# Kernel optimization log

Hardware: AMD Instinct MI355X
Metric: run time of the kernel (lower is better)

## Reference

```python
import jax, jax.numpy as jnp
import numpy as np

B, S, D, H, T = 512, 256, 64, 256, 50
IN = 2 * D + 1  # LSTM input dim = input_size*2+1
NSUB = 8       # RK4 substeps per output interval
TIME_OFFSET = 0.0

def _xavier(k, shape):
    fan_out, fan_in = shape
    lim = float(np.sqrt(6.0 / (fan_in + fan_out)))
    return jax.random.uniform(k, shape, minval=-lim, maxval=lim, dtype=jnp.float32)

def setup_inputs() -> dict:
    key = jax.random.key(0)
    ks = jax.random.split(key, 12)
    gaps = jax.random.uniform(ks[3], (B, T), minval=0.05, maxval=0.2, dtype=jnp.float32)
    return {
        "x": jax.random.normal(ks[0], (B, S, IN), jnp.float32),
        "lengths": jax.random.randint(ks[1], (B,), S // 2, S + 1),
        "label_feature": jax.random.normal(ks[2], (B, T, D), jnp.float32),
        "label_time": jnp.cumsum(gaps, axis=1),  # sorted per-sample times
        "label_mask": (jax.random.uniform(ks[4], (B, T, D)) < 0.2).astype(jnp.float32),
        "W_ih": _xavier(ks[5], (4 * H, IN)),
        "W_hh": _xavier(ks[6], (4 * H, H)),
        "b_ih": jnp.zeros((4 * H,), jnp.float32),
        "b_hh": jnp.zeros((4 * H,), jnp.float32),
        "Wp1": _xavier(ks[7], (H, H)), "bp1": jnp.zeros((H,), jnp.float32),
        "Wp2": _xavier(ks[8], (D, H)), "bp2": jnp.zeros((D,), jnp.float32),
        "Wd1": _xavier(ks[9], (H, D)), "bd1": jnp.zeros((H,), jnp.float32),
        "Wd2": _xavier(ks[10], (D, H)), "bd2": jnp.zeros((D,), jnp.float32),
    }

def _forward(x, label_feature, label_time, label_mask,
             W_ih, W_hh, b_ih, b_hh, Wp1, bp1, Wp2, bp2, Wd1, bd1, Wd2, bd2,
             lengths):
    # --- LSTM encoder (PyTorch gate order i, f, g, o) ---
    xW = jnp.einsum('bsi,gi->bsg', x, W_ih) + b_ih  # [B,S,4H]
    h0 = jnp.zeros((x.shape[0], H), x.dtype)
    def step(carry, xt):
        h, c = carry
        g = xt + h @ W_hh.T + b_hh
        i, f, gg, o = jnp.split(g, 4, axis=-1)
        c = jax.nn.sigmoid(f) * c + jax.nn.sigmoid(i) * jnp.tanh(gg)
        h = jax.nn.sigmoid(o) * jnp.tanh(c)
        return (h, c), h
    _, hs = jax.lax.scan(step, (h0, h0), jnp.swapaxes(xW, 0, 1))
    hs = jnp.swapaxes(hs, 0, 1)  # [B,S,H]
    # masked mean over valid timesteps
    mask = (jnp.arange(x.shape[1])[None, :] < lengths[:, None]).astype(x.dtype)
    pooled = (hs * mask[:, :, None]).sum(axis=1) / lengths[:, None].astype(x.dtype)
    # projection MLP -> initial ODE state
    y0 = jax.nn.relu(pooled @ Wp1.T + bp1) @ Wp2.T + bp2  # [B,D]
    # --- batched Neural-ODE integration (fixed-step RK4) ---
    def deriv(y):
        return jax.nn.relu(y @ Wd1.T + bd1) @ Wd2.T + bd2
    ts = label_time - TIME_OFFSET
    dts = (ts[:, 1:] - ts[:, :-1]) / NSUB  # [B,T-1]
    def interval(y, dt_b):
        dt = dt_b[:, None]
        for _ in range(NSUB):
            k1 = deriv(y)
            k2 = deriv(y + 0.5 * dt * k1)
            k3 = deriv(y + 0.5 * dt * k2)
            k4 = deriv(y + dt * k3)
            y = y + (dt / 6.0) * (k1 + 2.0 * k2 + 2.0 * k3 + k4)
        return y, y
    _, traj = jax.lax.scan(interval, y0, jnp.swapaxes(dts, 0, 1))  # [T-1,B,D]
    predict = jnp.swapaxes(jnp.concatenate([y0[None], traj], axis=0), 0, 1)  # [B,T,D]
    loss = (predict - label_feature) ** 2 * (1.0 - label_mask)
    return predict, loss

def reference(x, lengths, label_feature, label_time, label_mask,
              W_ih, W_hh, b_ih, b_hh, Wp1, bp1, Wp2, bp2, Wd1, bd1, Wd2, bd2):
    return _forward(x, label_feature, label_time, label_mask,
                    W_ih, W_hh, b_ih, b_hh, Wp1, bp1, Wp2, bp2, Wd1, bd1, Wd2, bd2,
                    lengths)
```

## Files before the change

kernel.cpp:

```cpp
#include <hip/hip_runtime.h>
#include <hip/hip_bf16.h>

#define BB 512
#define SS 256
#define HH 256
#define DD 64
#define TT 50
#define GG 1024
#define INW 129

typedef _Float16 h4 __attribute__((ext_vector_type(4)));
typedef _Float16 h8 __attribute__((ext_vector_type(8)));
typedef __fp16 hf2 __attribute__((ext_vector_type(2)));
typedef float f32x4 __attribute__((ext_vector_type(4)));
typedef unsigned int u32;

__device__ inline float sigf(float x) { return 1.f / (1.f + __expf(-x)); }
__device__ inline float tanhf_(float x) { return 1.f - 2.f / (__expf(2.f * x) + 1.f); }

__device__ inline u32 pkrtz(float a, float b) {
    hf2 h = __builtin_amdgcn_cvt_pkrtz(a, b);
    return __builtin_bit_cast(u32, h);
}
__device__ inline float fdot2u(u32 a, u32 b, float c) {
    return __builtin_amdgcn_fdot2(__builtin_bit_cast(hf2, a), __builtin_bit_cast(hf2, b), c, false);
}

__global__ __launch_bounds__(256) void prep_kernel(
    const float* __restrict__ W_hh, const float* __restrict__ W_ih,
    const float* __restrict__ Wd1, const float* __restrict__ Wd2,
    h4* __restrict__ BhhV4, h4* __restrict__ BhhL4, h4* __restrict__ BhhS4,
    _Float16* __restrict__ Bih, u32* __restrict__ Wd1p, u32* __restrict__ Wd2p)
{
    int idx = blockIdx.x * 256 + threadIdx.x;
    if (idx < 65536) {
        int eh = idx & 1;
        int l = (idx >> 1) & 63;
        int ks = (idx >> 7) & 7;
        int s = (idx >> 10) & 7;
        int w = (idx >> 13) & 7;
        int g = s & 3, jt = s >> 2;
        int n = g * 256 + w * 32 + jt * 16 + (l & 15);
        int k = 32 * ks + 8 * (l >> 4) + 4 * eh;
        float4 v = *(const float4*)(W_hh + (size_t)n * HH + k);
        h4 o; o[0] = (_Float16)v.x; o[1] = (_Float16)v.y; o[2] = (_Float16)v.z; o[3] = (_Float16)v.w;
        if (ks < 4)      BhhV4[(((w * 8 + s) * 4 + ks) * 64 + l) * 2 + eh] = o;
        else if (ks < 6) BhhL4[(((w * 8 + s) * 2 + (ks - 4)) * 64 + l) * 2 + eh] = o;
        else             BhhS4[(((w * 8 + s) * 2 + (ks - 6)) * 64 + l) * 2 + eh] = o;
    } else if (idx < 65536 + 40960) {
        int fj = idx - 65536;
        int eh = fj & 1;
        int l = (fj >> 1) & 63;
        int si = fj >> 7;
        int ks = si % 5;
        int ntile = si / 5;
        int n = ntile * 16 + (l & 15);
        int k = 32 * ks + 8 * (l >> 4) + 4 * eh;
        h4 o;
#pragma unroll
        for (int i = 0; i < 4; i++) {
            int kk = k + i;
            o[i] = (_Float16)((kk < INW) ? W_ih[(size_t)n * INW + kk] : 0.f);
        }
        *(h4*)(Bih + (size_t)fj * 4) = o;
    } else if (idx < 106496 + 8192) {
        int j2 = idx - 106496;
        int j = j2 >> 8, i = j2 & 255;
        Wd1p[j2] = pkrtz(Wd1[i * DD + 2 * j], Wd1[i * DD + 2 * j + 1]);
    } else if (idx < 114688 + 8192) {
        int j2 = idx - 114688;
        int j = j2 >> 8, t = j2 & 255;
        int o = ((t >> 6) << 4) + (t & 15);
        int q = (t >> 4) & 3;
        Wd2p[j2] = pkrtz(Wd2[(size_t)o * HH + q * 64 + 2 * j],
                         Wd2[(size_t)o * HH + q * 64 + 2 * j + 1]);
    }
}

__global__ __launch_bounds__(256) void xw_kernel(
    const float* __restrict__ x, const _Float16* __restrict__ Bih,
    const float* __restrict__ b_ih, const float* __restrict__ b_hh,
    h4* __restrict__ xwf)
{
    __shared__ __align__(16) _Float16 ash[4][5][64][8];
    int tid = threadIdx.x;
    int w4 = tid >> 6, l = tid & 63;
    int bx = blockIdx.x;
    int t = bx >> 3, Bb = bx & 7;

    for (int i = tid; i < 64 * 160; i += 256) {
        int rr = i / 160, kk = i % 160;
        float v = (kk < INW) ? x[((size_t)(Bb * 64 + rr) * SS + t) * INW + kk] : 0.f;
        ash[rr >> 4][kk >> 5][(((kk & 31) >> 3) << 4) + (rr & 15)][kk & 7] = (_Float16)v;
    }
    __syncthreads();

    h8 A[4][5];
#pragma unroll
    for (int ms = 0; ms < 4; ms++)
#pragma unroll
        for (int ks = 0; ks < 5; ks++)
            A[ms][ks] = *(h8*)&ash[ms][ks][l][0];

    const h8* Bih8 = (const h8*)Bih;
    for (int nt16 = 0; nt16 < 16; nt16++) {
        int ntile = w4 * 16 + nt16;
        h8 Bv[5];
#pragma unroll
        for (int ks = 0; ks < 5; ks++) Bv[ks] = Bih8[(ntile * 5 + ks) * 64 + l];
        int nb = ntile * 16 + (l & 15);
        float bias = b_ih[nb] + b_hh[nb];
        f32x4 acc[4];
#pragma unroll
        for (int ms = 0; ms < 4; ms++) acc[ms] = (f32x4){0.f, 0.f, 0.f, 0.f};
#pragma unroll
        for (int ks = 0; ks < 5; ks++)
#pragma unroll
            for (int ms = 0; ms < 4; ms++)
                acc[ms] = __builtin_amdgcn_mfma_f32_16x16x32_f16(A[ms][ks], Bv[ks], acc[ms], 0, 0, 0);
        int slot = ((ntile & 15) >> 1) * 8 + (ntile & 1) * 4 + (ntile >> 4);
#pragma unroll
        for (int ms = 0; ms < 4; ms++) {
            int bg = Bb * 4 + ms;
            h4 o;
#pragma unroll
            for (int r = 0; r < 4; r++) o[r] = (_Float16)(acc[ms][r] + bias);
            xwf[(((size_t)bg * SS + t) * 64 + slot) * 64 + l] = o;
        }
    }
}

__global__ __launch_bounds__(512, 2) void lstm_kernel(
    const h8* __restrict__ BhhV, const h8* __restrict__ BhhL, const h8* __restrict__ BhhS,
    const h4* __restrict__ xwf, const int* __restrict__ lengths, float* __restrict__ pooled)
{
    __shared__ __align__(16) _Float16 Wlds[65536];
    __shared__ __align__(16) _Float16 hbuf[2][8][64][8];
    int tid = threadIdx.x;
    int w = tid >> 6, l = tid & 63;
    int bg = blockIdx.x;

    {
        const uint4* src = (const uint4*)BhhL;
        uint4* dst = (uint4*)Wlds;
#pragma unroll
        for (int i = 0; i < 16; i++) dst[i * 512 + tid] = src[i * 512 + tid];
    }

    h8 Wv[8][4];
#pragma unroll
    for (int s = 0; s < 8; s++)
#pragma unroll
        for (int ks = 0; ks < 4; ks++)
            Wv[s][ks] = BhhV[((w * 8 + s) * 4 + ks) * 64 + l];

    int len_[4];
    float c_[2][4], pa[2][4];
#pragma unroll
    for (int r = 0; r < 4; r++) {
        int b = 4 * (l >> 4) + r;
        len_[r] = lengths[bg * 16 + b];
#pragma unroll
        for (int jt = 0; jt < 2; jt++) { c_[jt][r] = 0.f; pa[jt][r] = 0.f; }
    }

    {
        uint4* hz = (uint4*)hbuf;
        hz[tid] = make_uint4(0, 0, 0, 0);
        hz[512 + tid] = make_uint4(0, 0, 0, 0);
    }
    __syncthreads();

    int cur = 0;
    for (int t = 0; t < SS; t++) {
        const h4* xpb = xwf + (((size_t)bg * SS + t) * 64 + w * 8) * 64 + l;
        int zoff = 0;
        asm volatile("" : "+v"(zoff));
        const h8* bS = BhhS + zoff;
#pragma unroll
        for (int jt = 0; jt < 2; jt++) {
            h4 xv[4];
#pragma unroll
            for (int g = 0; g < 4; g++) xv[g] = xpb[(jt * 4 + g) * 64];
            h8 Ws[4];
#pragma unroll
            for (int g = 0; g < 4; g++) Ws[g] = bS[((w * 8 + jt * 4 + g) * 2 + 0) * 64 + l];
            f32x4 acc[4];
#pragma unroll
            for (int g = 0; g < 4; g++) acc[g] = (f32x4){0.f, 0.f, 0.f, 0.f};
#pragma unroll
            for (int ks = 0; ks < 4; ks++) {
                h8 A = *(const h8*)&hbuf[cur][ks][l][0];
#pragma unroll
                for (int g = 0; g < 4; g++)
                    acc[g] = __builtin_amdgcn_mfma_f32_16x16x32_f16(A, Wv[jt * 4 + g][ks], acc[g], 0, 0, 0);
            }
            {
                h8 A = *(const h8*)&hbuf[cur][6][l][0];
#pragma unroll
                for (int g = 0; g < 4; g++)
                    acc[g] = __builtin_amdgcn_mfma_f32_16x16x32_f16(A, Ws[g], acc[g], 0, 0, 0);
            }
#pragma unroll
            for (int g = 0; g < 4; g++) Ws[g] = bS[((w * 8 + jt * 4 + g) * 2 + 1) * 64 + l];
#pragma unroll
            for (int ks = 4; ks < 6; ks++) {
                h8 A = *(const h8*)&hbuf[cur][ks][l][0];
#pragma unroll
                for (int g = 0; g < 4; g++) {
                    h8 Bw = *(const h8*)&Wlds[(((w * 8 + jt * 4 + g) * 2 + (ks - 4)) * 64 + l) * 8];
                    acc[g] = __builtin_amdgcn_mfma_f32_16x16x32_f16(A, Bw, acc[g], 0, 0, 0);
                }
            }
            {
                h8 A = *(const h8*)&hbuf[cur][7][l][0];
#pragma unroll
                for (int g = 0; g < 4; g++)
                    acc[g] = __builtin_amdgcn_mfma_f32_16x16x32_f16(A, Ws[g], acc[g], 0, 0, 0);
            }
#pragma unroll
            for (int r = 0; r < 4; r++) {
                float gi = acc[0][r] + (float)xv[0][r];
                float gf = acc[1][r] + (float)xv[1][r];
                float gg = acc[2][r] + (float)xv[2][r];
                float go = acc[3][r] + (float)xv[3][r];
                float cc = sigf(gf) * c_[jt][r] + sigf(gi) * tanhf_(gg);
                c_[jt][r] = cc;
                float hh = sigf(go) * tanhf_(cc);
                if (t < len_[r]) pa[jt][r] += hh;
                int b = 4 * (l >> 4) + r;
                int j = w * 32 + jt * 16 + (l & 15);
                hbuf[cur ^ 1][j >> 5][(((j & 31) >> 3) << 4) + b][j & 7] = (_Float16)hh;
            }
        }
        __syncthreads();
        cur ^= 1;
    }

#pragma unroll
    for (int jt = 0; jt < 2; jt++)
#pragma unroll
        for (int r = 0; r < 4; r++) {
            int b = 4 * (l >> 4) + r;
            int j = w * 32 + jt * 16 + (l & 15);
            pooled[(size_t)(bg * 16 + b) * HH + j] = pa[jt][r] / (float)len_[r];
        }
}

__global__ __launch_bounds__(256) void head_kernel(
    const float* __restrict__ pooled, const float* __restrict__ Wp1,
    const float* __restrict__ bp1, const float* __restrict__ Wp2,
    const float* __restrict__ bp2, float* __restrict__ y0ws)
{
    __shared__ __align__(16) float psh[HH];
    __shared__ __align__(16) float rsh[HH];
    int tid = threadIdx.x, b = blockIdx.x;
    psh[tid] = pooled[(size_t)b * HH + tid];
    __syncthreads();
    float a = bp1[tid];
    const float* wr = Wp1 + (size_t)tid * HH;
#pragma unroll 8
    for (int k = 0; k < HH; k += 4) {
        float4 w = *(const float4*)(wr + k);
        a += psh[k] * w.x + psh[k + 1] * w.y + psh[k + 2] * w.z + psh[k + 3] * w.w;
    }
    rsh[tid] = fmaxf(a, 0.f);
    __syncthreads();
    if (tid < DD) {
        float acc = bp2[tid];
        const float* w2 = Wp2 + (size_t)tid * HH;
#pragma unroll 8
        for (int h = 0; h < HH; h += 4) {
            float4 w = *(const float4*)(w2 + h);
            acc += rsh[h] * w.x + rsh[h + 1] * w.y + rsh[h + 2] * w.z + rsh[h + 3] * w.w;
        }
        y0ws[(size_t)b * DD + tid] = acc;
    }
}

__global__ __launch_bounds__(256) void ode_kernel(
    const float* __restrict__ y0ws, const u32* __restrict__ Wd1p,
    const float* __restrict__ bd1, const u32* __restrict__ Wd2p,
    const float* __restrict__ bd2, const float* __restrict__ ltime,
    const float* __restrict__ lfeat, const float* __restrict__ lmask,
    float* __restrict__ pred, float* __restrict__ losso)
{
    __shared__ __align__(16) u32 ysh16[32];
    __shared__ __align__(16) u32 hsh16[128];
    int tid = threadIdx.x;
    int wv = tid >> 6, lq = tid & 63;
    int o = (wv << 4) + (lq & 15), q = lq >> 4;
    int b = blockIdx.x;
    u32 w1p[32], w2p[32];
#pragma unroll
    for (int j = 0; j < 32; j++) w1p[j] = Wd1p[j * 256 + tid];
#pragma unroll
    for (int j = 0; j < 32; j++) w2p[j] = Wd2p[j * 256 + tid];
    float bd1t = bd1[tid];
    float bd2o = bd2[o];
    float y = y0ws[(size_t)b * DD + o];
    if (q == 0) {
        size_t idx = ((size_t)b * TT + 0) * DD + o;
        pred[idx] = y;
        float lf = lfeat[idx], lm = lmask[idx];
        losso[idx] = (y - lf) * (y - lf) * (1.f - lm);
    }
    float kp = 0.f;
    for (int iv = 0; iv < TT - 1; iv++) {
        float t0 = ltime[(size_t)b * TT + iv], t1 = ltime[(size_t)b * TT + iv + 1];
        float dt = (t1 - t0) * 0.125f;
        for (int ss = 0; ss < 8; ss++) {
            float sacc = 0.f;
            kp = 0.f;
            const float AE[4] = {0.f, 0.5f, 0.5f, 1.f};
            const float WE[4] = {1.f, 2.f, 2.f, 1.f};
#pragma unroll
            for (int e = 0; e < 4; e++) {
                float yp = y + AE[e] * dt * kp;
                float ypo = __shfl_xor(yp, 1);
                if (lq < 16 && !(lq & 1))
                    ysh16[8 * wv + (lq >> 1)] = pkrtz(yp, ypo);
                __syncthreads();
                float a0 = 0.f, a1 = 0.f, a2 = 0.f, a3 = 0.f;
                const uint4* yv4 = (const uint4*)ysh16;
#pragma unroll
                for (int j4 = 0; j4 < 8; j4++) {
                    uint4 yv = yv4[j4];
                    a0 = fdot2u(w1p[4 * j4 + 0], yv.x, a0);
                    a1 = fdot2u(w1p[4 * j4 + 1], yv.y, a1);
                    a2 = fdot2u(w1p[4 * j4 + 2], yv.z, a2);
                    a3 = fdot2u(w1p[4 * j4 + 3], yv.w, a3);
                }
                float hv = fmaxf(bd1t + ((a0 + a1) + (a2 + a3)), 0.f);
                float hvo = __shfl_xor(hv, 1);
                if (!(tid & 1))
                    hsh16[tid >> 1] = pkrtz(hv, hvo);
                __syncthreads();
                float b0 = 0.f, b1 = 0.f, b2 = 0.f, b3 = 0.f;
                const uint4* hv4 = (const uint4*)&hsh16[q << 5];
#pragma unroll
                for (int j4 = 0; j4 < 8; j4++) {
                    uint4 hh = hv4[j4];
                    b0 = fdot2u(w2p[4 * j4 + 0], hh.x, b0);
                    b1 = fdot2u(w2p[4 * j4 + 1], hh.y, b1);
                    b2 = fdot2u(w2p[4 * j4 + 2], hh.z, b2);
                    b3 = fdot2u(w2p[4 * j4 + 3], hh.w, b3);
                }
                float p = (b0 + b1) + (b2 + b3);
                p += __shfl_xor(p, 16);
                p += __shfl_xor(p, 32);
                float kv = p + bd2o;
                kp = kv;
                sacc += WE[e] * kv;
            }
            y += dt * (1.f / 6.f) * sacc;
        }
        if (q == 0) {
            size_t idx = ((size_t)b * TT + iv + 1) * DD + o;
            pred[idx] = y;
            float lf = lfeat[idx], lm = lmask[idx];
            losso[idx] = (y - lf) * (y - lf) * (1.f - lm);
        }
    }
}

extern "C" void kernel_launch(void* const* d_in, const int* in_sizes, int n_in,
                              void* d_out, int out_size, void* d_ws, size_t ws_size,
                              hipStream_t stream)
{
    const float* x      = (const float*)d_in[0];
    const int* lengths  = (const int*)d_in[1];
    const float* lfeat  = (const float*)d_in[2];
    const float* ltime  = (const float*)d_in[3];
    const float* lmask  = (const float*)d_in[4];
    const float* W_ih   = (const float*)d_in[5];
    const float* W_hh   = (const float*)d_in[6];
    const float* b_ih   = (const float*)d_in[7];
    const float* b_hh   = (const float*)d_in[8];
    const float* Wp1    = (const float*)d_in[9];
    const float* bp1    = (const float*)d_in[10];
    const float* Wp2    = (const float*)d_in[11];
    const float* bp2    = (const float*)d_in[12];
    const float* Wd1    = (const float*)d_in[13];
    const float* bd1    = (const float*)d_in[14];
    const float* Wd2    = (const float*)d_in[15];
    const float* bd2    = (const float*)d_in[16];

    float* pred  = (float*)d_out;
    float* losso = pred + (size_t)BB * TT * DD;

    char* ws = (char*)d_ws;
    h4*       xwf    = (h4*)(ws + 0);
    h4*       BhhV   = (h4*)(ws + 268435456);
    h4*       BhhL   = (h4*)(ws + 268697600);
    h4*       BhhS   = (h4*)(ws + 268828672);
    _Float16* Bih    = (_Float16*)(ws + 268959744);
    float*    pooled = (float*)(ws + 269287424);
    float*    y0ws   = (float*)(ws + 269811712);
    u32*      Wd1p   = (u32*)(ws + 269942784);
    u32*      Wd2p   = (u32*)(ws + 269975552);

    prep_kernel<<<480, 256, 0, stream>>>(W_hh, W_ih, Wd1, Wd2, BhhV, BhhL, BhhS, Bih, Wd1p, Wd2p);
    xw_kernel<<<2048, 256, 0, stream>>>(x, Bih, b_ih, b_hh, xwf);
    lstm_kernel<<<32, 512, 0, stream>>>((const h8*)BhhV, (const h8*)BhhL, (const h8*)BhhS,
                                        xwf, lengths, pooled);
    head_kernel<<<BB, 256, 0, stream>>>(pooled, Wp1, bp1, Wp2, bp2, y0ws);
    ode_kernel<<<BB, 256, 0, stream>>>(y0ws, Wd1p, bd1, Wd2p, bd2, ltime, lfeat, lmask, pred, losso);
}
```

Measured before the change: 2.271 ms.

## Batch ODE RK4 over 16 samples with MFMA and prefetch LSTM inputs

The ODE kernel now handles 16 samples per block and runs both MLP layers with 16x16x32 fp16 MFMA instead of per-sample fdot2 loops. Weights are pre-swizzled into fragment layout by the prep kernel, and the hidden and derivative values are exchanged through XOR-swizzled LDS. The LSTM kernel prefetches the next timestep's input projection into registers, moves the h state to a swizzled row-major LDS layout, and loads both BhhS fragments up front. The ODE grid shrinks from 512 blocks to 32, which sharply lowers parallelism across the GPU's CUs in exchange for far more efficient matrix math. It also keeps more state in registers per thread.

New measurement: 2.673 ms. 1.18x slower.

```diff
diff --git a/kernel.cpp b/kernel.cpp
--- a/kernel.cpp
+++ b/kernel.cpp
@@ -22,15 +22,12 @@
     hf2 h = __builtin_amdgcn_cvt_pkrtz(a, b);
     return __builtin_bit_cast(u32, h);
 }
-__device__ inline float fdot2u(u32 a, u32 b, float c) {
-    return __builtin_amdgcn_fdot2(__builtin_bit_cast(hf2, a), __builtin_bit_cast(hf2, b), c, false);
-}
 
 __global__ __launch_bounds__(256) void prep_kernel(
     const float* __restrict__ W_hh, const float* __restrict__ W_ih,
     const float* __restrict__ Wd1, const float* __restrict__ Wd2,
     h4* __restrict__ BhhV4, h4* __restrict__ BhhL4, h4* __restrict__ BhhS4,
-    _Float16* __restrict__ Bih, u32* __restrict__ Wd1p, u32* __restrict__ Wd2p)
+    _Float16* __restrict__ Bih, h4* __restrict__ A1f4, h4* __restrict__ A2f4)
 {
     int idx = blockIdx.x * 256 + threadIdx.x;
     if (idx < 65536) {
@@ -47,7 +44,7 @@
         if (ks < 4)      BhhV4[(((w * 8 + s) * 4 + ks) * 64 + l) * 2 + eh] = o;
         else if (ks < 6) BhhL4[(((w * 8 + s) * 2 + (ks - 4)) * 64 + l) * 2 + eh] = o;
         else             BhhS4[(((w * 8 + s) * 2 + (ks - 6)) * 64 + l) * 2 + eh] = o;
-    } else if (idx < 65536 + 40960) {
+    } else if (idx < 106496) {
         int fj = idx - 65536;
         int eh = fj & 1;
         int l = (fj >> 1) & 63;
@@ -63,17 +60,30 @@
             o[i] = (_Float16)((kk < INW) ? W_ih[(size_t)n * INW + kk] : 0.f);
         }
         *(h4*)(Bih + (size_t)fj * 4) = o;
-    } else if (idx < 106496 + 8192) {
-        int j2 = idx - 106496;
-        int j = j2 >> 8, i = j2 & 255;
-        Wd1p[j2] = pkrtz(Wd1[i * DD + 2 * j], Wd1[i * DD + 2 * j + 1]);
-    } else if (idx < 114688 + 8192) {
-        int j2 = idx - 114688;
-        int j = j2 >> 8, t = j2 & 255;
-        int o = ((t >> 6) << 4) + (t & 15);
-        int q = (t >> 4) & 3;
-        Wd2p[j2] = pkrtz(Wd2[(size_t)o * HH + q * 64 + 2 * j],
-                         Wd2[(size_t)o * HH + q * 64 + 2 * j + 1]);
+    } else if (idx < 110592) {
+        int fj = idx - 106496;
+        int eh = fj & 1;
+        int l = (fj >> 1) & 63;
+        int slot = fj >> 7;
+        int ks = slot & 1, t = slot >> 1;
+        int row = 16 * t + (l & 15);
+        int k = 32 * ks + 8 * (l >> 4) + 4 * eh;
+        h4 o;
+#pragma unroll
+        for (int i = 0; i < 4; i++) o[i] = (_Float16)Wd1[(size_t)row * DD + k + i];
+        A1f4[fj] = o;
+    } else if (idx < 114688) {
+        int fj = idx - 110592;
+        int eh = fj & 1;
+        int l = (fj >> 1) & 63;
+        int slot = fj >> 7;
+        int ks = slot & 7, t2 = slot >> 3;
+        int row = 16 * t2 + (l & 15);
+        int k = 32 * ks + 8 * (l >> 4) + 4 * eh;
+        h4 o;
+#pragma unroll
+        for (int i = 0; i < 4; i++) o[i] = (_Float16)Wd2[(size_t)row * HH + k + i];
+        A2f4[fj] = o;
     }
 }
 
@@ -135,9 +145,10 @@
     const h4* __restrict__ xwf, const int* __restrict__ lengths, float* __restrict__ pooled)
 {
     __shared__ __align__(16) _Float16 Wlds[65536];
-    __shared__ __align__(16) _Float16 hbuf[2][8][64][8];
+    __shared__ __align__(16) _Float16 hst[2][4096];
     int tid = threadIdx.x;
     int w = tid >> 6, l = tid & 63;
+    int q = l >> 4, b0 = l & 15;
     int bg = blockIdx.x;
 
     {
@@ -158,54 +169,56 @@
     float c_[2][4], pa[2][4];
 #pragma unroll
     for (int r = 0; r < 4; r++) {
-        int b = 4 * (l >> 4) + r;
-        len_[r] = lengths[bg * 16 + b];
+        len_[r] = lengths[bg * 16 + 4 * q + r];
 #pragma unroll
         for (int jt = 0; jt < 2; jt++) { c_[jt][r] = 0.f; pa[jt][r] = 0.f; }
     }
 
     {
-        uint4* hz = (uint4*)hbuf;
+        uint4* hz = (uint4*)hst;
         hz[tid] = make_uint4(0, 0, 0, 0);
         hz[512 + tid] = make_uint4(0, 0, 0, 0);
     }
     __syncthreads();
 
+    h4 xc[8], xn[8];
+    {
+        const h4* p0 = xwf + (((size_t)bg * SS + 0) * 64 + w * 8) * 64 + l;
+#pragma unroll
+        for (int s = 0; s < 8; s++) xc[s] = p0[s * 64];
+    }
+
     int cur = 0;
     for (int t = 0; t < SS; t++) {
-        const h4* xpb = xwf + (((size_t)bg * SS + t) * 64 + w * 8) * 64 + l;
+        int tn = (t + 1) & 255;
+        const h4* pn = xwf + (((size_t)bg * SS + tn) * 64 + w * 8) * 64 + l;
+#pragma unroll
+        for (int s = 0; s < 8; s++) xn[s] = pn[s * 64];
+
         int zoff = 0;
         asm volatile("" : "+v"(zoff));
         const h8* bS = BhhS + zoff;
 #pragma unroll
         for (int jt = 0; jt < 2; jt++) {
-            h4 xv[4];
-#pragma unroll
-            for (int g = 0; g < 4; g++) xv[g] = xpb[(jt * 4 + g) * 64];
-            h8 Ws[4];
-#pragma unroll
-            for (int g = 0; g < 4; g++) Ws[g] = bS[((w * 8 + jt * 4 + g) * 2 + 0) * 64 + l];
+            h8 Ws[8];
+#pragma unroll
+            for (int g = 0; g < 4; g++) {
+                Ws[g]     = bS[((w * 8 + jt * 4 + g) * 2 + 0) * 64 + l];
+                Ws[4 + g] = bS[((w * 8 + jt * 4 + g) * 2 + 1) * 64 + l];
+            }
             f32x4 acc[4];
 #pragma unroll
             for (int g = 0; g < 4; g++) acc[g] = (f32x4){0.f, 0.f, 0.f, 0.f};
 #pragma unroll
             for (int ks = 0; ks < 4; ks++) {
-                h8 A = *(const h8*)&hbuf[cur][ks][l][0];
+                h8 A = *(const h8*)&hst[cur][(b0 * 256 + 32 * ks + 8 * q) ^ ((b0 & 7) << 3)];
 #pragma unroll
                 for (int g = 0; g < 4; g++)
                     acc[g] = __builtin_amdgcn_mfma_f32_16x16x32_f16(A, Wv[jt * 4 + g][ks], acc[g], 0, 0, 0);
             }
-            {
-                h8 A = *(const h8*)&hbuf[cur][6][l][0];
-#pragma unroll
-                for (int g = 0; g < 4; g++)
-                    acc[g] = __builtin_amdgcn_mfma_f32_16x16x32_f16(A, Ws[g], acc[g], 0, 0, 0);
-            }
-#pragma unroll
-            for (int g = 0; g < 4; g++) Ws[g] = bS[((w * 8 + jt * 4 + g) * 2 + 1) * 64 + l];
 #pragma unroll
             for (int ks = 4; ks < 6; ks++) {
-                h8 A = *(const h8*)&hbuf[cur][ks][l][0];
+                h8 A = *(const h8*)&hst[cur][(b0 * 256 + 32 * ks + 8 * q) ^ ((b0 & 7) << 3)];
 #pragma unroll
                 for (int g = 0; g < 4; g++) {
                     h8 Bw = *(const h8*)&Wlds[(((w * 8 + jt * 4 + g) * 2 + (ks - 4)) * 64 + l) * 8];
@@ -213,27 +226,35 @@
                 }
             }
             {
-                h8 A = *(const h8*)&hbuf[cur][7][l][0];
+                h8 A = *(const h8*)&hst[cur][(b0 * 256 + 32 * 6 + 8 * q) ^ ((b0 & 7) << 3)];
 #pragma unroll
                 for (int g = 0; g < 4; g++)
                     acc[g] = __builtin_amdgcn_mfma_f32_16x16x32_f16(A, Ws[g], acc[g], 0, 0, 0);
             }
+            {
+                h8 A = *(const h8*)&hst[cur][(b0 * 256 + 32 * 7 + 8 * q) ^ ((b0 & 7) << 3)];
+#pragma unroll
+                for (int g = 0; g < 4; g++)
+                    acc[g] = __builtin_amdgcn_mfma_f32_16x16x32_f16(A, Ws[4 + g], acc[g], 0, 0, 0);
+            }
 #pragma unroll
             for (int r = 0; r < 4; r++) {
-                float gi = acc[0][r] + (float)xv[0][r];
-                float gf = acc[1][r] + (float)xv[1][r];
-                float gg = acc[2][r] + (float)xv[2][r];
-                float go = acc[3][r] + (float)xv[3][r];
+                float gi = acc[0][r] + (float)xc[jt * 4 + 0][r];
+                float gf = acc[1][r] + (float)xc[jt * 4 + 1][r];
+                float gg = acc[2][r] + (float)xc[jt * 4 + 2][r];
+                float go = acc[3][r] + (float)xc[jt * 4 + 3][r];
                 float cc = sigf(gf) * c_[jt][r] + sigf(gi) * tanhf_(gg);
                 c_[jt][r] = cc;
                 float hh = sigf(go) * tanhf_(cc);
                 if (t < len_[r]) pa[jt][r] += hh;
-                int b = 4 * (l >> 4) + r;
-                int j = w * 32 + jt * 16 + (l & 15);
-                hbuf[cur ^ 1][j >> 5][(((j & 31) >> 3) << 4) + b][j & 7] = (_Float16)hh;
+                int b = 4 * q + r;
+                int j = w * 32 + jt * 16 + b0;
+                hst[cur ^ 1][(b * 256 + j) ^ ((b & 7) << 3)] = (_Float16)hh;
             }
         }
         __syncthreads();
+#pragma unroll
+        for (int s = 0; s < 8; s++) xc[s] = xn[s];
         cur ^= 1;
     }
 
@@ -241,8 +262,8 @@
     for (int jt = 0; jt < 2; jt++)
 #pragma unroll
         for (int r = 0; r < 4; r++) {
-            int b = 4 * (l >> 4) + r;
-            int j = w * 32 + jt * 16 + (l & 15);
+            int b = 4 * q + r;
+            int j = w * 32 + jt * 16 + b0;
             pooled[(size_t)(bg * 16 + b) * HH + j] = pa[jt][r] / (float)len_[r];
         }
 }
@@ -279,87 +300,165 @@
 }
 
 __global__ __launch_bounds__(256) void ode_kernel(
-    const float* __restrict__ y0ws, const u32* __restrict__ Wd1p,
-    const float* __restrict__ bd1, const u32* __restrict__ Wd2p,
+    const float* __restrict__ y0ws, const h8* __restrict__ A1f,
+    const float* __restrict__ bd1, const h8* __restrict__ A2f,
     const float* __restrict__ bd2, const float* __restrict__ ltime,
     const float* __restrict__ lfeat, const float* __restrict__ lmask,
     float* __restrict__ pred, float* __restrict__ losso)
 {
-    __shared__ __align__(16) u32 ysh16[32];
-    __shared__ __align__(16) u32 hsh16[128];
+    __shared__ __align__(16) _Float16 hX[4096];
+    __shared__ __align__(16) _Float16 kX[1024];
     int tid = threadIdx.x;
-    int wv = tid >> 6, lq = tid & 63;
-    int o = (wv << 4) + (lq & 15), q = lq >> 4;
-    int b = blockIdx.x;
-    u32 w1p[32], w2p[32];
-#pragma unroll
-    for (int j = 0; j < 32; j++) w1p[j] = Wd1p[j * 256 + tid];
-#pragma unroll
-    for (int j = 0; j < 32; j++) w2p[j] = Wd2p[j * 256 + tid];
-    float bd1t = bd1[tid];
-    float bd2o = bd2[o];
-    float y = y0ws[(size_t)b * DD + o];
-    if (q == 0) {
-        size_t idx = ((size_t)b * TT + 0) * DD + o;
-        pred[idx] = y;
-        float lf = lfeat[idx], lm = lmask[idx];
-        losso[idx] = (y - lf) * (y - lf) * (1.f - lm);
-    }
-    float kp = 0.f;
+    int wv = tid >> 6, l = tid & 63;
+    int q = l >> 4, bb = l & 15;
+    int b = blockIdx.x * 16 + bb;
+
+    h8 A1[4][2];
+#pragma unroll
+    for (int tt = 0; tt < 4; tt++)
+#pragma unroll
+        for (int ks = 0; ks < 2; ks++)
+            A1[tt][ks] = A1f[((4 * wv + tt) * 2 + ks) * 64 + l];
+    h8 A2[8];
+#pragma unroll
+    for (int ks = 0; ks < 8; ks++) A2[ks] = A2f[(wv * 8 + ks) * 64 + l];
+
+    float bd1c[4][4];
+#pragma unroll
+    for (int tt = 0; tt < 4; tt++)
+#pragma unroll
+        for (int r = 0; r < 4; r++) bd1c[tt][r] = bd1[16 * (4 * wv + tt) + 4 * q + r];
+    float bd2c[4];
+#pragma unroll
+    for (int r = 0; r < 4; r++) bd2c[r] = bd2[16 * wv + 4 * q + r];
+
+    float y[16], kp[16], ksum[16];
+#pragma unroll
+    for (int ks = 0; ks < 2; ks++)
+#pragma unroll
+        for (int e = 0; e < 8; e++) {
+            y[ks * 8 + e] = y0ws[(size_t)b * DD + 32 * ks + 8 * q + e];
+            kp[ks * 8 + e] = 0.f;
+        }
+
+    if (wv == 0) {
+#pragma unroll
+        for (int ks = 0; ks < 2; ks++) {
+            size_t idx = ((size_t)b * TT + 0) * DD + 32 * ks + 8 * q;
+            float4 p0 = make_float4(y[ks * 8 + 0], y[ks * 8 + 1], y[ks * 8 + 2], y[ks * 8 + 3]);
+            float4 p1 = make_float4(y[ks * 8 + 4], y[ks * 8 + 5], y[ks * 8 + 6], y[ks * 8 + 7]);
+            *(float4*)&pred[idx] = p0;
+            *(float4*)&pred[idx + 4] = p1;
+            float4 lf0 = *(const float4*)&lfeat[idx], lf1 = *(const float4*)&lfeat[idx + 4];
+            float4 lm0 = *(const float4*)&lmask[idx], lm1 = *(const float4*)&lmask[idx + 4];
+            float4 lo0, lo1;
+            lo0.x = (p0.x - lf0.x) * (p0.x - lf0.x) * (1.f - lm0.x);
+            lo0.y = (p0.y - lf0.y) * (p0.y - lf0.y) * (1.f - lm0.y);
+            lo0.z = (p0.z - lf0.z) * (p0.z - lf0.z) * (1.f - lm0.z);
+            lo0.w = (p0.w - lf0.w) * (p0.w - lf0.w) * (1.f - lm0.w);
+            lo1.x = (p1.x - lf1.x) * (p1.x - lf1.x) * (1.f - lm1.x);
+            lo1.y = (p1.y - lf1.y) * (p1.y - lf1.y) * (1.f - lm1.y);
+            lo1.z = (p1.z - lf1.z) * (p1.z - lf1.z) * (1.f - lm1.z);
+            lo1.w = (p1.w - lf1.w) * (p1.w - lf1.w) * (1.f - lm1.w);
+            *(float4*)&losso[idx] = lo0;
+            *(float4*)&losso[idx + 4] = lo1;
+        }
+    }
+
     for (int iv = 0; iv < TT - 1; iv++) {
         float t0 = ltime[(size_t)b * TT + iv], t1 = ltime[(size_t)b * TT + iv + 1];
         float dt = (t1 - t0) * 0.125f;
         for (int ss = 0; ss < 8; ss++) {
-            float sacc = 0.f;
-            kp = 0.f;
+#pragma unroll
+            for (int i = 0; i < 16; i++) ksum[i] = 0.f;
             const float AE[4] = {0.f, 0.5f, 0.5f, 1.f};
             const float WE[4] = {1.f, 2.f, 2.f, 1.f};
 #pragma unroll
             for (int e = 0; e < 4; e++) {
-                float yp = y + AE[e] * dt * kp;
-                float ypo = __shfl_xor(yp, 1);
-                if (lq < 16 && !(lq & 1))
-                    ysh16[8 * wv + (lq >> 1)] = pkrtz(yp, ypo);
+                h8 B1[2];
+#pragma unroll
+                for (int ks = 0; ks < 2; ks++) {
+                    float ye[8];
+#pragma unroll
+                    for (int i = 0; i < 8; i++) ye[i] = y[ks * 8 + i] + AE[e] * dt * kp[ks * 8 + i];
+                    uint4 u;
+                    u.x = pkrtz(ye[0], ye[1]); u.y = pkrtz(ye[2], ye[3]);
+                    u.z = pkrtz(ye[4], ye[5]); u.w = pkrtz(ye[6], ye[7]);
+                    B1[ks] = __builtin_bit_cast(h8, u);
+                }
+                f32x4 C1[4];
+#pragma unroll
+                for (int tt = 0; tt < 4; tt++) C1[tt] = (f32x4){0.f, 0.f, 0.f, 0.f};
+#pragma unroll
+                for (int ks = 0; ks < 2; ks++)
+#pragma unroll
+                    for (int tt = 0; tt < 4; tt++)
+                        C1[tt] = __builtin_amdgcn_mfma_f32_16x16x32_f16(A1[tt][ks], B1[ks], C1[tt], 0, 0, 0);
+#pragma unroll
+                for (int tt = 0; tt < 4; tt++) {
+                    float h0 = fmaxf(C1[tt][0] + bd1c[tt][0], 0.f);
+                    float h1 = fmaxf(C1[tt][1] + bd1c[tt][1], 0.f);
+                    float h2 = fmaxf(C1[tt][2] + bd1c[tt][2], 0.f);
+                    float h3 = fmaxf(C1[tt][3] + bd1c[tt][3], 0.f);
+                    int i0 = 16 * (4 * wv + tt) + 4 * q;
+                    int idx = (bb * 256 + i0) ^ ((bb & 7) << 3);
+                    *(uint2*)&hX[idx] = make_uint2(pkrtz(h0, h1), pkrtz(h2, h3));
+                }
                 __syncthreads();
-                float a0 = 0.f, a1 = 0.f, a2 = 0.f, a3 = 0.f;
-                const uint4* yv4 = (const uint4*)ysh16;
-#pragma unroll
-                for (int j4 = 0; j4 < 8; j4++) {
-                    uint4 yv = yv4[j4];
-                    a0 = fdot2u(w1p[4 * j4 + 0], yv.x, a0);
-                    a1 = fdot2u(w1p[4 * j4 + 1], yv.y, a1);
-                    a2 = fdot2u(w1p[4 * j4 + 2], yv.z, a2);
-                    a3 = fdot2u(w1p[4 * j4 + 3], yv.w, a3);
+                f32x4 Ca = (f32x4){0.f, 0.f, 0.f, 0.f}, Cb = (f32x4){0.f, 0.f, 0.f, 0.f};
+#pragma unroll
+                for (int ks = 0; ks < 8; ks += 2) {
+                    h8 B2a = *(const h8*)&hX[(bb * 256 + 32 * ks + 8 * q) ^ ((bb & 7) << 3)];
+                    h8 B2b = *(const h8*)&hX[(bb * 256 + 32 * (ks + 1) + 8 * q) ^ ((bb & 7) << 3)];
+                    Ca = __builtin_amdgcn_mfma_f32_16x16x32_f16(A2[ks], B2a, Ca, 0, 0, 0);
+                    Cb = __builtin_amdgcn_mfma_f32_16x16x32_f16(A2[ks + 1], B2b, Cb, 0, 0, 0);
                 }
-                float hv = fmaxf(bd1t + ((a0 + a1) + (a2 + a3)), 0.f);
-                float hvo = __shfl_xor(hv, 1);
-                if (!(tid & 1))
-                    hsh16[tid >> 1] = pkrtz(hv, hvo);
+                {
+                    float k0 = Ca[0] + Cb[0] + bd2c[0];
+                    float k1 = Ca[1] + Cb[1] + bd2c[1];
+                    float k2 = Ca[2] + Cb[2] + bd2c[2];
+                    float k3 = Ca[3] + Cb[3] + bd2c[3];
+                    int j0 = 16 * wv + 4 * q;
+                    int idx = (bb * 64 + j0) ^ ((bb & 7) << 3);
+                    *(uint2*)&kX[idx] = make_uint2(pkrtz(k0, k1), pkrtz(k2, k3));
+                }
                 __syncthreads();
-                float b0 = 0.f, b1 = 0.f, b2 = 0.f, b3 = 0.f;
-                const uint4* hv4 = (const uint4*)&hsh16[q << 5];
-#pragma unroll
-                for (int j4 = 0; j4 < 8; j4++) {
-                    uint4 hh = hv4[j4];
-                    b0 = fdot2u(w2p[4 * j4 + 0], hh.x, b0);
-                    b1 = fdot2u(w2p[4 * j4 + 1], hh.y, b1);
-                    b2 = fdot2u(w2p[4 * j4 + 2], hh.z, b2);
-                    b3 = fdot2u(w2p[4 * j4 + 3], hh.w, b3);
+#pragma unroll
+                for (int ks = 0; ks < 2; ks++) {
+                    h8 kvh = *(const h8*)&kX[(bb * 64 + 32 * ks + 8 * q) ^ ((bb & 7) << 3)];
+#pragma unroll
+                    for (int i = 0; i < 8; i++) {
+                        float kvf = (float)kvh[i];
+                        kp[ks * 8 + i] = kvf;
+                        ksum[ks * 8 + i] += WE[e] * kvf;
+                    }
                 }
-                float p = (b0 + b1) + (b2 + b3);
-                p += __shfl_xor(p, 16);
-                p += __shfl_xor(p, 32);
-                float kv = p + bd2o;
-                kp = kv;
-                sacc += WE[e] * kv;
-            }
-            y += dt * (1.f / 6.f) * sacc;
-        }
-        if (q == 0) {
-            size_t idx = ((size_t)b * TT + iv + 1) * DD + o;
-            pred[idx] = y;
-            float lf = lfeat[idx], lm = lmask[idx];
-            losso[idx] = (y - lf) * (y - lf) * (1.f - lm);
+            }
+#pragma unroll
+            for (int i = 0; i < 16; i++) y[i] += dt * (1.f / 6.f) * ksum[i];
+        }
+        if (wv == 0) {
+#pragma unroll
+            for (int ks = 0; ks < 2; ks++) {
+                size_t idx = ((size_t)b * TT + iv + 1) * DD + 32 * ks + 8 * q;
+                float4 p0 = make_float4(y[ks * 8 + 0], y[ks * 8 + 1], y[ks * 8 + 2], y[ks * 8 + 3]);
+                float4 p1 = make_float4(y[ks * 8 + 4], y[ks * 8 + 5], y[ks * 8 + 6], y[ks * 8 + 7]);
+                *(float4*)&pred[idx] = p0;
+                *(float4*)&pred[idx + 4] = p1;
+                float4 lf0 = *(const float4*)&lfeat[idx], lf1 = *(const float4*)&lfeat[idx + 4];
+                float4 lm0 = *(const float4*)&lmask[idx], lm1 = *(const float4*)&lmask[idx + 4];
+                float4 lo0, lo1;
+                lo0.x = (p0.x - lf0.x) * (p0.x - lf0.x) * (1.f - lm0.x);
+                lo0.y = (p0.y - lf0.y) * (p0.y - lf0.y) * (1.f - lm0.y);
+                lo0.z = (p0.z - lf0.z) * (p0.z - lf0.z) * (1.f - lm0.z);
+                lo0.w = (p0.w - lf0.w) * (p0.w - lf0.w) * (1.f - lm0.w);
+                lo1.x = (p1.x - lf1.x) * (p1.x - lf1.x) * (1.f - lm1.x);
+                lo1.y = (p1.y - lf1.y) * (p1.y - lf1.y) * (1.f - lm1.y);
+                lo1.z = (p1.z - lf1.z) * (p1.z - lf1.z) * (1.f - lm1.z);
+                lo1.w = (p1.w - lf1.w) * (p1.w - lf1.w) * (1.f - lm1.w);
+                *(float4*)&losso[idx] = lo0;
+                *(float4*)&losso[idx + 4] = lo1;
+            }
         }
     }
 }
@@ -397,13 +496,14 @@
     _Float16* Bih    = (_Float16*)(ws + 268959744);
     float*    pooled = (float*)(ws + 269287424);
     float*    y0ws   = (float*)(ws + 269811712);
-    u32*      Wd1p   = (u32*)(ws + 269942784);
-    u32*      Wd2p   = (u32*)(ws + 269975552);
-
-    prep_kernel<<<480, 256, 0, stream>>>(W_hh, W_ih, Wd1, Wd2, BhhV, BhhL, BhhS, Bih, Wd1p, Wd2p);
+    h4*       A1f    = (h4*)(ws + 269942784);
+    h4*       A2f    = (h4*)(ws + 269975552);
+
+    prep_kernel<<<448, 256, 0, stream>>>(W_hh, W_ih, Wd1, Wd2, BhhV, BhhL, BhhS, Bih, A1f, A2f);
     xw_kernel<<<2048, 256, 0, stream>>>(x, Bih, b_ih, b_hh, xwf);
     lstm_kernel<<<32, 512, 0, stream>>>((const h8*)BhhV, (const h8*)BhhL, (const h8*)BhhS,
                                         xwf, lengths, pooled);
     head_kernel<<<BB, 256, 0, stream>>>(pooled, Wp1, bp1, Wp2, bp2, y0ws);
-    ode_kernel<<<BB, 256, 0, stream>>>(y0ws, Wd1p, bd1, Wd2p, bd2, ltime, lfeat, lmask, pred, losso);
-}
+    ode_kernel<<<32, 256, 0, stream>>>(y0ws, (const h8*)A1f, bd1, (const h8*)A2f, bd2,
+                                       ltime, lfeat, lmask, pred, losso);
+}
```
